# Kernel tuning notes

Hardware: AMD Instinct MI355X
Metric: run time of the kernel (lower is better)

Reference implementation:

```python
import jax, jax.numpy as jnp
import numpy as np

B, SEQ, DIM = 1, 2048, 4096
N_HEADS, N_KV, HEAD_DIM = 32, 8, 128
N_REP = N_HEADS // N_KV
MAX_CTX = 4096


def setup_inputs() -> dict:
    key = jax.random.key(0)
    ks = jax.random.split(key, 6)
    x = jax.random.normal(ks[0], (B, SEQ, DIM), jnp.float32)
    # RoPE table: (1, SEQ, 1, HEAD_DIM//2, 2) with [cos, sin] in last dim
    inv_freq = 1.0 / (10000.0 ** (jnp.arange(0, HEAD_DIM, 2, dtype=jnp.float32) / HEAD_DIM))
    t = jnp.arange(SEQ, dtype=jnp.float32)
    ang = t[:, None] * inv_freq[None, :]
    freqs_cis = jnp.stack([jnp.cos(ang), jnp.sin(ang)], axis=-1).reshape(1, SEQ, 1, HEAD_DIM // 2, 2)
    cache_kv = jnp.zeros((2, 1, MAX_CTX, N_KV, HEAD_DIM), jnp.float32)
    s = 0.02
    wq = jax.random.normal(ks[1], (DIM, N_HEADS * HEAD_DIM), jnp.float32) * s
    wk = jax.random.normal(ks[2], (DIM, N_KV * HEAD_DIM), jnp.float32) * s
    wv = jax.random.normal(ks[3], (DIM, N_KV * HEAD_DIM), jnp.float32) * s
    wo = jax.random.normal(ks[4], (N_HEADS * HEAD_DIM, DIM), jnp.float32) * s
    return {"x": x, "cache_kv": cache_kv, "freqs_cis": freqs_cis,
            "wq": wq, "wk": wk, "wv": wv, "wo": wo, "start_pos": 0}


def _rope(t, freqs_cis):
    # t: (b, s, h, head_dim); freqs_cis: (1, s, 1, head_dim//2, 2)
    tr = t.reshape(*t.shape[:-1], -1, 2)
    a, b = tr[..., 0], tr[..., 1]
    c, d = freqs_cis[..., 0], freqs_cis[..., 1]
    return jnp.stack([a * c - b * d, a * d + b * c], axis=-1).reshape(t.shape)


def reference(x, cache_kv, freqs_cis, wq, wk, wv, wo, start_pos):
    b, s, _ = x.shape
    xq = (x @ wq).reshape(b, s, N_HEADS, HEAD_DIM)
    xk = (x @ wk).reshape(b, s, N_KV, HEAD_DIM)
    xv = (x @ wv).reshape(b, s, N_KV, HEAD_DIM)
    xq = _rope(xq, freqs_cis)
    xk = _rope(xk, freqs_cis)
    # KV-cache scatter write (start_pos is a static Python int)
    cache = cache_kv.at[:, :, start_pos:start_pos + s].set(jnp.stack([xk, xv]))
    L = start_pos + s
    keys = cache[0, :, :L]    # (b, L, kv, hd)
    values = cache[1, :, :L]
    # GQA without materializing repeats: group q heads by kv head
    q = xq.transpose(0, 2, 1, 3).reshape(b, N_KV, N_REP, s, HEAD_DIM)
    k = keys.transpose(0, 2, 1, 3)     # (b, kv, L, hd)
    v = values.transpose(0, 2, 1, 3)
    scores = jnp.einsum('bkrqd,bkld->bkrql', q, k) * (HEAD_DIM ** -0.5)
    if s > 1:
        mask = jnp.triu(jnp.full((s, L), -jnp.inf, jnp.float32), k=start_pos + 1)
        scores = scores + mask
    p = jax.nn.softmax(scores, axis=-1)
    out = jnp.einsum('bkrql,bkld->bkrqd', p, v)          # (b, kv, rep, s, hd)
    out = out.reshape(b, N_HEADS, s, HEAD_DIM).transpose(0, 2, 1, 3).reshape(b, s, N_HEADS * HEAD_DIM)
    return out @ wo
```

## Files before the change

### kernel.cpp

```cpp
#include <hip/hip_runtime.h>
#include <hip/hip_bf16.h>
#include <stdint.h>

#define SEQ   2048
#define DIM   4096
#define NH    32
#define NKV   8
#define HD    128
#define NREP  4
#define QKVN  6144
#define KOFF  4096
#define VOFF  5120

typedef __bf16 bf16;
typedef __attribute__((ext_vector_type(8))) __bf16 bf16x8;
typedef __attribute__((ext_vector_type(4))) __bf16 bf16x4;
typedef __attribute__((ext_vector_type(4))) float  f32x4;
typedef __attribute__((address_space(1))) void as1_void;
typedef __attribute__((address_space(3))) void as3_void;

__device__ __forceinline__ void async_copy16(void* lds, const void* g) {
  __builtin_amdgcn_global_load_lds((as1_void*)(void*)g, (as3_void*)lds, 16, 0, 0);
}

__device__ __forceinline__ uint32_t pack2bf(float a, float b) {
  union { bf16 h; uint16_t u; } ca, cb;
  ca.h = (bf16)a; cb.h = (bf16)b;
  return (uint32_t)ca.u | ((uint32_t)cb.u << 16);
}

__global__ __launch_bounds__(256) void cast_x_kernel(const float* __restrict__ src,
                                                     bf16* __restrict__ dst) {
  size_t i = ((size_t)blockIdx.x * 256 + threadIdx.x) * 4;
  const float4 v = *(const float4*)(src + i);
  bf16x4 o;
  o[0] = (bf16)v.x; o[1] = (bf16)v.y; o[2] = (bf16)v.z; o[3] = (bf16)v.w;
  *(bf16x4*)(dst + i) = o;
}

__global__ __launch_bounds__(256) void transpose_cast_kernel(const float* __restrict__ src,
                                                             bf16* __restrict__ dst,
                                                             int R, int C) {
  __shared__ float tile[32][33];
  int c0 = blockIdx.x * 32, r0 = blockIdx.y * 32;
  int tx = threadIdx.x & 31, ty = threadIdx.x >> 5;
#pragma unroll
  for (int j = 0; j < 4; ++j)
    tile[ty + j*8][tx] = src[(size_t)(r0 + ty + j*8) * C + c0 + tx];
  __syncthreads();
#pragma unroll
  for (int j = 0; j < 4; ++j)
    dst[(size_t)(c0 + ty + j*8) * R + r0 + tx] = (bf16)tile[tx][ty + j*8];
}

template<int OUT_F32>
__global__ __launch_bounds__(256) void gemm_bt_kernel(const bf16* __restrict__ A,
                                                      const bf16* __restrict__ Bt,
                                                      void* __restrict__ Cout,
                                                      int M, int N, int K) {
  __shared__ __align__(16) bf16 As[128*32];
  __shared__ __align__(16) bf16 Bs[128*32];
  const int tid = threadIdx.x;
  const int w = tid >> 6, lane = tid & 63;
  const int lane16 = lane & 15, quad = lane >> 4;
  const int wr = w >> 1, wc = w & 1;
  const int bm = blockIdx.y * 128, bn = blockIdx.x * 128;
  const bf16* a0 = A  + (size_t)bm * K;
  const bf16* b0 = Bt + (size_t)bn * K;
  f32x4 acc[4][4] = {};
  for (int k0 = 0; k0 < K; k0 += 32) {
    __syncthreads();
#pragma unroll
    for (int i = 0; i < 2; ++i) {
      int c = tid + i * 256;
      async_copy16(&As[c*8], a0 + (size_t)(c >> 2) * K + k0 + (c & 3) * 8);
      async_copy16(&Bs[c*8], b0 + (size_t)(c >> 2) * K + k0 + (c & 3) * 8);
    }
    __syncthreads();
    bf16x8 af[4];
#pragma unroll
    for (int i = 0; i < 4; ++i)
      af[i] = *(const bf16x8*)&As[(wr*64 + i*16 + lane16)*32 + quad*8];
#pragma unroll
    for (int j = 0; j < 4; ++j) {
      bf16x8 bfrag = *(const bf16x8*)&Bs[(wc*64 + j*16 + lane16)*32 + quad*8];
#pragma unroll
      for (int i = 0; i < 4; ++i)
        acc[i][j] = __builtin_amdgcn_mfma_f32_16x16x32_bf16(af[i], bfrag, acc[i][j], 0, 0, 0);
    }
  }
#pragma unroll
  for (int i = 0; i < 4; ++i)
#pragma unroll
    for (int j = 0; j < 4; ++j)
#pragma unroll
      for (int r = 0; r < 4; ++r) {
        size_t row = (size_t)bm + wr*64 + i*16 + quad*4 + r;
        size_t col = (size_t)bn + wc*64 + j*16 + lane16;
        float v = acc[i][j][r];
        if (OUT_F32) ((float*)Cout)[row * N + col] = v;
        else         ((bf16*)Cout)[row * N + col] = (bf16)v;
      }
}

__global__ __launch_bounds__(256) void rope_kernel(bf16* __restrict__ qkv,
                                                   const float* __restrict__ fr) {
  int idx = blockIdx.x * 256 + threadIdx.x;
  int p  = idx & 63;
  int hh = (idx >> 6) % 40;
  int t  = (idx >> 6) / 40;
  int col = (hh < NH) ? (hh * HD + 2*p) : (KOFF + (hh - NH) * HD + 2*p);
  float c = fr[((size_t)t*64 + p)*2 + 0];
  float d = fr[((size_t)t*64 + p)*2 + 1];
  bf16* ptr = qkv + (size_t)t * QKVN + col;
  float a = (float)ptr[0], b = (float)ptr[1];
  ptr[0] = (bf16)(a*c - b*d);
  ptr[1] = (bf16)(a*d + b*c);
}

__global__ __launch_bounds__(256) void transpose_v_kernel(const bf16* __restrict__ qkv,
                                                          bf16* __restrict__ vt) {
  __shared__ bf16 tile[32][33];
  int tt = blockIdx.x * 32;
  int dd = blockIdx.y * 32;
  int kv = blockIdx.z;
  int tx = threadIdx.x & 31, ty = threadIdx.x >> 5;
  const bf16* src = qkv + VOFF + kv * HD;
#pragma unroll
  for (int j = 0; j < 4; ++j)
    tile[ty + j*8][tx] = src[(size_t)(tt + ty + j*8) * QKVN + dd + tx];
  __syncthreads();
  bf16* dst = vt + ((size_t)kv * HD + dd) * SEQ + tt;
#pragma unroll
  for (int j = 0; j < 4; ++j)
    dst[(size_t)(ty + j*8) * SEQ + tx] = tile[tx][ty + j*8];
}

__global__ __launch_bounds__(256, 3) void flash_attn_kernel(const bf16* __restrict__ qkv,
                                                            const bf16* __restrict__ vt,
                                                            bf16* __restrict__ out) {
  __shared__ __align__(16) bf16 Qs[64*HD];
  __shared__ __align__(16) bf16 Ks[64*HD];
  __shared__ __align__(16) bf16 Vts[64*HD];
  const int b  = blockIdx.x;
  const int qt = 31 - (b >> 5);
  const int h  = b & 31;
  const int kvh = h >> 2;
  const int tid = threadIdx.x;
  const int w = tid >> 6, lane = tid & 63;
  const int lane16 = lane & 15, quad = lane >> 4;
  const float scale = 0.08838834764831845f;
  const int qglob = qt*64 + w*16 + lane16;

  const bf16* qbase = qkv + (size_t)(qt*64) * QKVN + h * HD;
#pragma unroll
  for (int i = 0; i < 4; ++i) {
    int c = tid + i * 256;
    int kk = c >> 8, cp = c & 255;
    async_copy16(&Qs[c*8], qbase + (size_t)(cp >> 2) * QKVN + kk*32 + (cp & 3) * 8);
  }

  f32x4 acc_o[8] = {};
  float m_s = -3e38f, l_s = 0.f;

  const bf16* kbase0 = qkv + KOFF + kvh * HD;
  const bf16* vbase0 = vt + (size_t)kvh * HD * SEQ;

  for (int j = 0; j <= qt; ++j) {
    const int kv0 = j * 64;
    __syncthreads();
#pragma unroll
    for (int i = 0; i < 4; ++i) {
      int c = tid + i * 256;
      {
        int kk = c >> 8, cp = c & 255;
        async_copy16(&Ks[c*8], kbase0 + (size_t)(kv0 + (cp >> 2)) * QKVN + kk*32 + (cp & 3) * 8);
      }
      {
        int kk2 = c >> 9, cp = c & 511;
        async_copy16(&Vts[c*8], vbase0 + (size_t)(cp >> 2) * SEQ + kv0 + kk2*32 + (cp & 3) * 8);
      }
    }
    __syncthreads();

    f32x4 accT[4] = {};
#pragma unroll
    for (int kk = 0; kk < 4; ++kk) {
      bf16x8 qf = *(const bf16x8*)&Qs[(kk*64 + w*16 + lane16)*32 + quad*8];
#pragma unroll
      for (int jn = 0; jn < 4; ++jn) {
        bf16x8 kf = *(const bf16x8*)&Ks[(kk*64 + jn*16 + lane16)*32 + quad*8];
        accT[jn] = __builtin_amdgcn_mfma_f32_16x16x32_bf16(kf, qf, accT[jn], 0, 0, 0);
      }
    }

    float s[4][4];
#pragma unroll
    for (int jn = 0; jn < 4; ++jn)
#pragma unroll
      for (int r = 0; r < 4; ++r) {
        float v = accT[jn][r] * scale;
        if (j == qt && (kv0 + jn*16 + quad*4 + r) > qglob) v = -3e38f;
        s[jn][r] = v;
      }

    float mt = s[0][0];
#pragma unroll
    for (int jn = 0; jn < 4; ++jn)
#pragma unroll
      for (int r = 0; r < 4; ++r) mt = fmaxf(mt, s[jn][r]);
    mt = fmaxf(mt, __shfl_xor(mt, 16));
    mt = fmaxf(mt, __shfl_xor(mt, 32));
    float mnew = fmaxf(m_s, mt);
    float alpha = __expf(m_s - mnew);
    m_s = mnew;
    float rs = 0.f;
#pragma unroll
    for (int jn = 0; jn < 4; ++jn)
#pragma unroll
      for (int r = 0; r < 4; ++r) {
        float p = __expf(s[jn][r] - mnew);
        s[jn][r] = p;
        rs += p;
      }
    rs += __shfl_xor(rs, 16);
    rs += __shfl_xor(rs, 32);
    l_s = l_s * alpha + rs;

    float alpha_row[4];
#pragma unroll
    for (int r = 0; r < 4; ++r)
      alpha_row[r] = __shfl(alpha, quad*4 + r);
#pragma unroll
    for (int jd = 0; jd < 8; ++jd)
#pragma unroll
      for (int r = 0; r < 4; ++r) acc_o[jd][r] *= alpha_row[r];

    uint32_t pk[4][2];
#pragma unroll
    for (int jn = 0; jn < 4; ++jn) {
      pk[jn][0] = pack2bf(s[jn][0], s[jn][1]);
      pk[jn][1] = pack2bf(s[jn][2], s[jn][3]);
    }

    const int src0 = (quad & 1) * 32 + lane16;
    const int src1 = src0 + 16;
    const bool hi = quad >= 2;
#pragma unroll
    for (int kk2 = 0; kk2 < 2; ++kk2) {
      uint32_t v0l = __shfl(pk[2*kk2][0],   src0), v0h = __shfl(pk[2*kk2][1],   src0);
      uint32_t v1l = __shfl(pk[2*kk2][0],   src1), v1h = __shfl(pk[2*kk2][1],   src1);
      uint32_t w0l = __shfl(pk[2*kk2+1][0], src0), w0h = __shfl(pk[2*kk2+1][1], src0);
      uint32_t w1l = __shfl(pk[2*kk2+1][0], src1), w1h = __shfl(pk[2*kk2+1][1], src1);
      union { uint32_t u[4]; bf16x8 v; } af;
      af.u[0] = hi ? w0l : v0l;
      af.u[1] = hi ? w0h : v0h;
      af.u[2] = hi ? w1l : v1l;
      af.u[3] = hi ? w1h : v1h;
#pragma unroll
      for (int jd = 0; jd < 8; ++jd) {
        bf16x8 vf = *(const bf16x8*)&Vts[(kk2*128 + jd*16 + lane16)*32 + quad*8];
        acc_o[jd] = __builtin_amdgcn_mfma_f32_16x16x32_bf16(af.v, vf, acc_o[jd], 0, 0, 0);
      }
    }
  }

  const float inv_l = 1.f / l_s;
  float linv[4];
#pragma unroll
  for (int r = 0; r < 4; ++r)
    linv[r] = __shfl(inv_l, quad*4 + r);

  bf16* obase = out + (size_t)(qt*64 + w*16) * DIM + h * HD;
#pragma unroll
  for (int jd = 0; jd < 8; ++jd)
#pragma unroll
    for (int r = 0; r < 4; ++r)
      obase[(size_t)(quad*4 + r) * DIM + jd*16 + lane16] = (bf16)(acc_o[jd][r] * linv[r]);
}

extern "C" void kernel_launch(void* const* d_in, const int* in_sizes, int n_in,
                              void* d_out, int out_size, void* d_ws, size_t ws_size,
                              hipStream_t stream) {
  const float* x  = (const float*)d_in[0];
  const float* fr = (const float*)d_in[2];
  const float* wq = (const float*)d_in[3];
  const float* wk = (const float*)d_in[4];
  const float* wv = (const float*)d_in[5];
  const float* wo = (const float*)d_in[6];
  float* out = (float*)d_out;

  char* ws = (char*)d_ws;
  bf16* xb     = (bf16*)(ws);
  bf16* wqkv_t = (bf16*)(ws + 16777216);
  bf16* wo_t   = (bf16*)(ws + 67108864);
  bf16* qkv    = (bf16*)(ws + 100663296);
  bf16* vt     = (bf16*)(ws + 125829120);
  bf16* attn   = (bf16*)(ws + 130023424);
  (void)ws_size; (void)in_sizes; (void)n_in; (void)out_size;

  cast_x_kernel<<<8192, 256, 0, stream>>>(x, xb);
  transpose_cast_kernel<<<dim3(128,128), 256, 0, stream>>>(wq, wqkv_t, DIM, DIM);
  transpose_cast_kernel<<<dim3(32,128),  256, 0, stream>>>(wk, wqkv_t + (size_t)4096*4096, DIM, 1024);
  transpose_cast_kernel<<<dim3(32,128),  256, 0, stream>>>(wv, wqkv_t + (size_t)5120*4096, DIM, 1024);
  transpose_cast_kernel<<<dim3(128,128), 256, 0, stream>>>(wo, wo_t, DIM, DIM);

  gemm_bt_kernel<0><<<dim3(48,16), 256, 0, stream>>>(xb, wqkv_t, qkv, SEQ, QKVN, DIM);
  rope_kernel<<<20480, 256, 0, stream>>>(qkv, fr);
  transpose_v_kernel<<<dim3(64,4,8), 256, 0, stream>>>(qkv, vt);
  flash_attn_kernel<<<1024, 256, 0, stream>>>(qkv, vt, attn);
  gemm_bt_kernel<1><<<dim3(32,16), 256, 0, stream>>>(attn, wo_t, out, SEQ, DIM, DIM);
}
```

Baseline: 565.6 us.

## Hold Q in registers, widen attention KV tile to 96, pack transpose stores

The flash attention kernel now keeps Q fragments in registers instead of LDS. It processes keys and values in tiles of 96 rather than 64, and applies the causal mask on every tile instead of only the diagonal one. The transpose-cast kernel writes two packed bf16 values per store. The goal is fewer loop iterations and barriers, lower LDS use for better occupancy, and wider stores, at the cost of more registers, per-tile mask work, and wasted compute on partially masked tiles.

```diff
diff --git a/kernel.cpp b/kernel.cpp
--- a/kernel.cpp
+++ b/kernel.cpp
@@ -48,9 +48,15 @@
   for (int j = 0; j < 4; ++j)
     tile[ty + j*8][tx] = src[(size_t)(r0 + ty + j*8) * C + c0 + tx];
   __syncthreads();
-#pragma unroll
-  for (int j = 0; j < 4; ++j)
-    dst[(size_t)(c0 + ty + j*8) * R + r0 + tx] = (bf16)tile[tx][ty + j*8];
+  int g = threadIdx.x >> 4;
+  int k = threadIdx.x & 15;
+#pragma unroll
+  for (int jj = 0; jj < 2; ++jj) {
+    int X  = g + jj*16;
+    int Y0 = k*2;
+    uint32_t pv = pack2bf(tile[Y0][X], tile[Y0+1][X]);
+    *(uint32_t*)&dst[(size_t)(c0 + X) * R + r0 + Y0] = pv;
+  }
 }
 
 template<int OUT_F32>
@@ -139,9 +145,8 @@
 __global__ __launch_bounds__(256, 3) void flash_attn_kernel(const bf16* __restrict__ qkv,
                                                             const bf16* __restrict__ vt,
                                                             bf16* __restrict__ out) {
-  __shared__ __align__(16) bf16 Qs[64*HD];
-  __shared__ __align__(16) bf16 Ks[64*HD];
-  __shared__ __align__(16) bf16 Vts[64*HD];
+  __shared__ __align__(16) bf16 Ks[4*96*32];
+  __shared__ __align__(16) bf16 Vts[3*128*32];
   const int b  = blockIdx.x;
   const int qt = 31 - (b >> 5);
   const int h  = b & 31;
@@ -152,13 +157,11 @@
   const float scale = 0.08838834764831845f;
   const int qglob = qt*64 + w*16 + lane16;
 
-  const bf16* qbase = qkv + (size_t)(qt*64) * QKVN + h * HD;
-#pragma unroll
-  for (int i = 0; i < 4; ++i) {
-    int c = tid + i * 256;
-    int kk = c >> 8, cp = c & 255;
-    async_copy16(&Qs[c*8], qbase + (size_t)(cp >> 2) * QKVN + kk*32 + (cp & 3) * 8);
-  }
+  const bf16* qrow = qkv + (size_t)qglob * QKVN + h * HD + quad*8;
+  bf16x8 qreg[4];
+#pragma unroll
+  for (int kk = 0; kk < 4; ++kk)
+    qreg[kk] = *(const bf16x8*)(qrow + kk*32);
 
   f32x4 acc_o[8] = {};
   float m_s = -3e38f, l_s = 0.f;
@@ -166,15 +169,16 @@
   const bf16* kbase0 = qkv + KOFF + kvh * HD;
   const bf16* vbase0 = vt + (size_t)kvh * HD * SEQ;
 
-  for (int j = 0; j <= qt; ++j) {
-    const int kv0 = j * 64;
+  const int L = (qt*64 + 159) / 96;
+  for (int jj = 0; jj < L; ++jj) {
+    const int kv0 = jj * 96;
     __syncthreads();
 #pragma unroll
-    for (int i = 0; i < 4; ++i) {
+    for (int i = 0; i < 6; ++i) {
       int c = tid + i * 256;
       {
-        int kk = c >> 8, cp = c & 255;
-        async_copy16(&Ks[c*8], kbase0 + (size_t)(kv0 + (cp >> 2)) * QKVN + kk*32 + (cp & 3) * 8);
+        int kk = c / 384, rem = c - kk*384;
+        async_copy16(&Ks[c*8], kbase0 + (size_t)(kv0 + (rem >> 2)) * QKVN + kk*32 + (rem & 3) * 8);
       }
       {
         int kk2 = c >> 9, cp = c & 511;
@@ -183,30 +187,28 @@
     }
     __syncthreads();
 
-    f32x4 accT[4] = {};
-#pragma unroll
-    for (int kk = 0; kk < 4; ++kk) {
-      bf16x8 qf = *(const bf16x8*)&Qs[(kk*64 + w*16 + lane16)*32 + quad*8];
-#pragma unroll
-      for (int jn = 0; jn < 4; ++jn) {
-        bf16x8 kf = *(const bf16x8*)&Ks[(kk*64 + jn*16 + lane16)*32 + quad*8];
-        accT[jn] = __builtin_amdgcn_mfma_f32_16x16x32_bf16(kf, qf, accT[jn], 0, 0, 0);
-      }
-    }
-
-    float s[4][4];
-#pragma unroll
-    for (int jn = 0; jn < 4; ++jn)
+    f32x4 accT[6] = {};
+#pragma unroll
+    for (int kk = 0; kk < 4; ++kk)
+#pragma unroll
+      for (int jn = 0; jn < 6; ++jn) {
+        bf16x8 kf = *(const bf16x8*)&Ks[(kk*96 + jn*16 + lane16)*32 + quad*8];
+        accT[jn] = __builtin_amdgcn_mfma_f32_16x16x32_bf16(kf, qreg[kk], accT[jn], 0, 0, 0);
+      }
+
+    float s[6][4];
+#pragma unroll
+    for (int jn = 0; jn < 6; ++jn)
 #pragma unroll
       for (int r = 0; r < 4; ++r) {
         float v = accT[jn][r] * scale;
-        if (j == qt && (kv0 + jn*16 + quad*4 + r) > qglob) v = -3e38f;
+        if ((kv0 + jn*16 + quad*4 + r) > qglob) v = -3e38f;
         s[jn][r] = v;
       }
 
     float mt = s[0][0];
 #pragma unroll
-    for (int jn = 0; jn < 4; ++jn)
+    for (int jn = 0; jn < 6; ++jn)
 #pragma unroll
       for (int r = 0; r < 4; ++r) mt = fmaxf(mt, s[jn][r]);
     mt = fmaxf(mt, __shfl_xor(mt, 16));
@@ -216,7 +218,7 @@
     m_s = mnew;
     float rs = 0.f;
 #pragma unroll
-    for (int jn = 0; jn < 4; ++jn)
+    for (int jn = 0; jn < 6; ++jn)
 #pragma unroll
       for (int r = 0; r < 4; ++r) {
         float p = __expf(s[jn][r] - mnew);
@@ -236,9 +238,9 @@
 #pragma unroll
       for (int r = 0; r < 4; ++r) acc_o[jd][r] *= alpha_row[r];
 
-    uint32_t pk[4][2];
-#pragma unroll
-    for (int jn = 0; jn < 4; ++jn) {
+    uint32_t pk[6][2];
+#pragma unroll
+    for (int jn = 0; jn < 6; ++jn) {
       pk[jn][0] = pack2bf(s[jn][0], s[jn][1]);
       pk[jn][1] = pack2bf(s[jn][2], s[jn][3]);
     }
@@ -247,7 +249,7 @@
     const int src1 = src0 + 16;
     const bool hi = quad >= 2;
 #pragma unroll
-    for (int kk2 = 0; kk2 < 2; ++kk2) {
+    for (int kk2 = 0; kk2 < 3; ++kk2) {
       uint32_t v0l = __shfl(pk[2*kk2][0],   src0), v0h = __shfl(pk[2*kk2][1],   src0);
       uint32_t v1l = __shfl(pk[2*kk2][0],   src1), v1h = __shfl(pk[2*kk2][1],   src1);
       uint32_t w0l = __shfl(pk[2*kk2+1][0], src0), w0h = __shfl(pk[2*kk2+1][1], src0);
```

After: 569.8 us. Within noise of the previous version (+0.7%).
